# Kernel tuning notes

Measured on AMD Instinct MI355X. Metric: run time of the kernel, lower is better.

Reference implementation:

```python
import jax, jax.numpy as jnp
import numpy as np

L = 4           # num_layers
H = 1536        # hidden_size
NQ = 12         # num_q_heads
NKV = 2         # num_kv_heads
D = 128         # head_dim
I = 8960        # mlp intermediate
S = 2048        # q_len == max_seq_len (full prefill, past_kv_len = 0)
EPS = 1e-6
SCALE = 1.0 / np.sqrt(D)


def setup_inputs() -> dict:
    key = jax.random.key(0)
    ks = jax.random.split(key, 16)
    hidden_states = jax.random.normal(ks[0], (1, S, H), dtype=jnp.float32)
    # real RoPE tables (base 10000), duplicated-half layout like HF Qwen2
    inv_freq = 1.0 / (10000.0 ** (np.arange(0, D, 2, dtype=np.float32) / D))
    t = np.arange(S, dtype=np.float32)
    freqs = np.outer(t, inv_freq)                      # [S, D/2]
    emb = np.concatenate([freqs, freqs], axis=-1)      # [S, D]
    position_cos = jnp.asarray(np.cos(emb))[None]      # [1, S, D]
    position_sin = jnp.asarray(np.sin(emb))[None]
    # causal additive mask [1, 1, S, S]
    causal = jnp.tril(jnp.ones((S, S), dtype=bool))
    attention_mask = jnp.where(causal, 0.0, -1e9).astype(jnp.float32)[None, None]
    sd = 0.02
    Wq = sd * jax.random.normal(ks[1], (L, H, NQ * D), dtype=jnp.float32)
    bq = jnp.zeros((L, NQ * D), dtype=jnp.float32)
    Wk = sd * jax.random.normal(ks[2], (L, H, NKV * D), dtype=jnp.float32)
    bk = jnp.zeros((L, NKV * D), dtype=jnp.float32)
    Wv = sd * jax.random.normal(ks[3], (L, H, NKV * D), dtype=jnp.float32)
    bv = jnp.zeros((L, NKV * D), dtype=jnp.float32)
    Wo = sd * jax.random.normal(ks[4], (L, NQ * D, H), dtype=jnp.float32)
    Wgate = sd * jax.random.normal(ks[5], (L, H, I), dtype=jnp.float32)
    Wup = sd * jax.random.normal(ks[6], (L, H, I), dtype=jnp.float32)
    Wdown = sd * jax.random.normal(ks[7], (L, I, H), dtype=jnp.float32)
    ln1_w = jnp.ones((L, H), dtype=jnp.float32)
    ln2_w = jnp.ones((L, H), dtype=jnp.float32)
    final_ln_w = jnp.ones((H,), dtype=jnp.float32)
    return dict(hidden_states=hidden_states, position_cos=position_cos,
                position_sin=position_sin, attention_mask=attention_mask,
                Wq=Wq, bq=bq, Wk=Wk, bk=bk, Wv=Wv, bv=bv, Wo=Wo,
                Wgate=Wgate, Wup=Wup, Wdown=Wdown,
                ln1_w=ln1_w, ln2_w=ln2_w, final_ln_w=final_ln_w)


def rms_norm(x, w):
    return x * jax.lax.rsqrt(jnp.mean(x * x, axis=-1, keepdims=True) + EPS) * w


def rotate_half(x):
    x1, x2 = jnp.split(x, 2, axis=-1)
    return jnp.concatenate([-x2, x1], axis=-1)


def reference(hidden_states, position_cos, position_sin, attention_mask,
              Wq, bq, Wk, bk, Wv, bv, Wo, Wgate, Wup, Wdown,
              ln1_w, ln2_w, final_ln_w):
    cos = position_cos[:, None]  # [1, 1, S, D]
    sin = position_sin[:, None]
    x = hidden_states
    rep = NQ // NKV
    for i in range(L):
        residual = x
        h = rms_norm(x, ln1_w[i])
        q = (h @ Wq[i] + bq[i]).reshape(1, S, NQ, D).transpose(0, 2, 1, 3)   # [1,NQ,S,D]
        k = (h @ Wk[i] + bk[i]).reshape(1, S, NKV, D).transpose(0, 2, 1, 3)  # [1,NKV,S,D]
        v = (h @ Wv[i] + bv[i]).reshape(1, S, NKV, D).transpose(0, 2, 1, 3)
        q = q * cos + rotate_half(q) * sin
        k = k * cos + rotate_half(k) * sin
        # KV cache write is fp16; full prefill so cache == current k/v (fp16 roundtrip)
        k_full = k.astype(jnp.float16).astype(jnp.float32)
        v_full = v.astype(jnp.float16).astype(jnp.float32)
        k_full = jnp.repeat(k_full, rep, axis=1)  # GQA expand -> [1,NQ,S,D]
        v_full = jnp.repeat(v_full, rep, axis=1)
        scores = jnp.einsum('bhqd,bhkd->bhqk', q, k_full) * SCALE + attention_mask
        probs = jax.nn.softmax(scores, axis=-1)
        attn = jnp.einsum('bhqk,bhkd->bhqd', probs, v_full)
        attn = attn.transpose(0, 2, 1, 3).reshape(1, S, NQ * D)
        x = residual + attn @ Wo[i]
        residual = x
        h = rms_norm(x, ln2_w[i])
        x = residual + (jax.nn.silu(h @ Wgate[i]) * (h @ Wup[i])) @ Wdown[i]
    return rms_norm(x, final_ln_w)
```

## Files before the change

kernel.cpp:

```cpp
#include <hip/hip_runtime.h>

#define S_LEN 2048
#define H_DIM 1536
#define NQ_H 12
#define NKV_H 2
#define HD 128
#define I_DIM 8960
#define QKV_N 2048
#define GU_N 17920
#define SCALE 0.08838834764831845f

typedef _Float16 f16;
typedef _Float16 f16x8 __attribute__((ext_vector_type(8)));
typedef float f32x4 __attribute__((ext_vector_type(4)));

__device__ __forceinline__ void gload16(const void* g, void* l) {
  __builtin_amdgcn_global_load_lds((__attribute__((address_space(1))) void*)g,
                                   (__attribute__((address_space(3))) void*)l,
                                   16, 0, 0);
}

template <int MODE>
__global__ __launch_bounds__(256) void gemm_bt(const f16* __restrict__ A,
                                               const f16* __restrict__ BT,
                                               float* __restrict__ Cf,
                                               f16* __restrict__ Ch,
                                               int M, int N, int K) {
  __shared__ __attribute__((aligned(16))) f16 As[128 * 32];
  __shared__ __attribute__((aligned(16))) f16 Bs[128 * 32];
  const int tid = threadIdx.x;
  const int w = tid >> 6, lane = tid & 63;
  const int quad = lane >> 4, cc = lane & 15;
  const int wm = w >> 1, wn = w & 1;
  const int m0 = blockIdx.y * 128, n0 = blockIdx.x * 128;

  const int c1 = tid, c2 = tid + 256;
  const f16* Ag1 = A + (size_t)(m0 + (c1 >> 2)) * K + (c1 & 3) * 8;
  const f16* Ag2 = A + (size_t)(m0 + (c2 >> 2)) * K + (c2 & 3) * 8;
  const f16* Bg1 = BT + (size_t)(n0 + (c1 >> 2)) * K + (c1 & 3) * 8;
  const f16* Bg2 = BT + (size_t)(n0 + (c2 >> 2)) * K + (c2 & 3) * 8;
  f16* Al1 = As + (w * 64) * 8;
  f16* Al2 = As + (256 + w * 64) * 8;
  f16* Bl1 = Bs + (w * 64) * 8;
  f16* Bl2 = Bs + (256 + w * 64) * 8;

  const f32x4 fz = {0.f, 0.f, 0.f, 0.f};
  f32x4 acc[4][4];
#pragma unroll
  for (int i = 0; i < 4; ++i)
#pragma unroll
    for (int j = 0; j < 4; ++j) acc[i][j] = fz;

  for (int k0 = 0; k0 < K; k0 += 32) {
    __syncthreads();
    gload16(Ag1 + k0, Al1);
    gload16(Ag2 + k0, Al2);
    gload16(Bg1 + k0, Bl1);
    gload16(Bg2 + k0, Bl2);
    __syncthreads();
    f16x8 af[4], bf[4];
#pragma unroll
    for (int i = 0; i < 4; ++i)
      af[i] = *(const f16x8*)(As + (wm * 64 + i * 16 + cc) * 32 + quad * 8);
#pragma unroll
    for (int j = 0; j < 4; ++j)
      bf[j] = *(const f16x8*)(Bs + (wn * 64 + j * 16 + cc) * 32 + quad * 8);
#pragma unroll
    for (int i = 0; i < 4; ++i)
#pragma unroll
      for (int j = 0; j < 4; ++j)
        acc[i][j] = __builtin_amdgcn_mfma_f32_16x16x32_f16(af[i], bf[j], acc[i][j], 0, 0, 0);
  }

#pragma unroll
  for (int i = 0; i < 4; ++i) {
    const int row = m0 + wm * 64 + i * 16 + quad * 4;
#pragma unroll
    for (int j = 0; j < 4; ++j) {
      const int col = n0 + wn * 64 + j * 16 + cc;
#pragma unroll
      for (int r = 0; r < 4; ++r) {
        const size_t idx = (size_t)(row + r) * N + col;
        if (MODE == 0) Cf[idx] = acc[i][j][r];
        else if (MODE == 1) Cf[idx] += acc[i][j][r];
        else Ch[idx] = (f16)acc[i][j][r];
      }
    }
  }
}

__global__ __launch_bounds__(256) void transpose_f2h(const float* __restrict__ src,
                                                     f16* __restrict__ dst,
                                                     int K_, int N_) {
  __shared__ float tile[32][33];
  const int c0 = blockIdx.x * 32, r0 = blockIdx.y * 32;
  const int x = threadIdx.x & 31, y4 = threadIdx.x >> 5;
#pragma unroll
  for (int i = 0; i < 4; ++i) {
    int r = r0 + y4 + i * 8;
    if (r < K_ && c0 + x < N_) tile[y4 + i * 8][x] = src[(size_t)r * N_ + c0 + x];
  }
  __syncthreads();
#pragma unroll
  for (int i = 0; i < 4; ++i) {
    int rr = y4 + i * 8;
    int dr = c0 + rr, dc = r0 + x;
    if (dr < N_ && dc < K_) dst[(size_t)dr * K_ + dc] = (f16)tile[x][rr];
  }
}

template <bool OUT_F32>
__global__ __launch_bounds__(256) void rmsnorm_kernel(const float* __restrict__ x,
                                                      const float* __restrict__ w,
                                                      f16* __restrict__ hh,
                                                      float* __restrict__ hf) {
  const int s = blockIdx.x;
  const float* xr = x + (size_t)s * H_DIM;
  float ss = 0.f;
  for (int i = threadIdx.x; i < H_DIM; i += 256) {
    float v = xr[i];
    ss += v * v;
  }
#pragma unroll
  for (int m = 32; m >= 1; m >>= 1) ss += __shfl_xor(ss, m);
  __shared__ float red[4];
  if ((threadIdx.x & 63) == 0) red[threadIdx.x >> 6] = ss;
  __syncthreads();
  ss = red[0] + red[1] + red[2] + red[3];
  const float rr = rsqrtf(ss * (1.0f / H_DIM) + 1e-6f);
  for (int i = threadIdx.x; i < H_DIM; i += 256) {
    float v = xr[i] * rr * w[i];
    if (OUT_F32) hf[(size_t)s * H_DIM + i] = v;
    else hh[(size_t)s * H_DIM + i] = (f16)v;
  }
}

__global__ __launch_bounds__(256) void rope_kernel(const float* __restrict__ qkv,
                                                   const float* __restrict__ cosb,
                                                   const float* __restrict__ sinb,
                                                   const float* __restrict__ bq,
                                                   const float* __restrict__ bk,
                                                   const float* __restrict__ bv,
                                                   f16* __restrict__ q_r,
                                                   f16* __restrict__ k_r,
                                                   f16* __restrict__ v_r) {
  const int s = blockIdx.x;
  const float* row = qkv + (size_t)s * QKV_N;
#pragma unroll
  for (int ci = 0; ci < 8; ++ci) {
    const int col = ci * 256 + threadIdx.x;
    if (col < 1536) {
      const int hh = col >> 7, d = col & 127;
      const int part = (d < 64) ? d + 64 : d - 64;
      const float v0 = row[col] + bq[col];
      const float v1 = row[(hh << 7) + part] + bq[(hh << 7) + part];
      const float cs = cosb[s * HD + d], sn = sinb[s * HD + d];
      const float rot = (d < 64) ? -v1 : v1;
      q_r[((size_t)hh * S_LEN + s) * HD + d] = (f16)(v0 * cs + rot * sn);
    } else if (col < 1792) {
      const int cc2 = col - 1536;
      const int hh = cc2 >> 7, d = cc2 & 127;
      const int part = (d < 64) ? d + 64 : d - 64;
      const float v0 = row[col] + bk[cc2];
      const float v1 = row[1536 + (hh << 7) + part] + bk[(hh << 7) + part];
      const float cs = cosb[s * HD + d], sn = sinb[s * HD + d];
      const float rot = (d < 64) ? -v1 : v1;
      k_r[((size_t)hh * S_LEN + s) * HD + d] = (f16)(v0 * cs + rot * sn);
    } else {
      const int cc2 = col - 1792;
      const int hh = cc2 >> 7, d = cc2 & 127;
      const float v0 = row[col] + bv[cc2];
      v_r[((size_t)hh * HD + d) * S_LEN + s] = (f16)v0;
    }
  }
}

__global__ __launch_bounds__(256) void attn_kernel(const f16* __restrict__ Q,
                                                   const f16* __restrict__ Kc,
                                                   const f16* __restrict__ Vt,
                                                   f16* __restrict__ Oa) {
  __shared__ __attribute__((aligned(16))) f16 ks[64 * 136];
  __shared__ __attribute__((aligned(16))) f16 vs[128 * 72];
  __shared__ __attribute__((aligned(16))) f16 ps[128 * 72];
  const int h = blockIdx.x, qt = blockIdx.y;
  const int hk = h / (NQ_H / NKV_H);
  const int tid = threadIdx.x, w = tid >> 6, lane = tid & 63;
  const int quad = lane >> 4, cc = lane & 15;

  f16x8 qf[2][4];
  const f16* Qg = Q + ((size_t)h * S_LEN + qt * 128) * HD;
#pragma unroll
  for (int i = 0; i < 2; ++i)
#pragma unroll
    for (int kk = 0; kk < 4; ++kk)
      qf[i][kk] = *(const f16x8*)(Qg + (size_t)(w * 32 + i * 16 + cc) * HD + kk * 32 + quad * 8);

  const f32x4 fz = {0.f, 0.f, 0.f, 0.f};
  f32x4 o_acc[2][8];
  float m_run[2][4], l_run[2][4];
#pragma unroll
  for (int i = 0; i < 2; ++i) {
#pragma unroll
    for (int j = 0; j < 8; ++j) o_acc[i][j] = fz;
#pragma unroll
    for (int r = 0; r < 4; ++r) { m_run[i][r] = -1e30f; l_run[i][r] = 0.f; }
  }

  const int nkt = 2 * qt + 2;
  for (int kt = 0; kt < nkt; ++kt) {
    const int kv0 = kt * 64;
    __syncthreads();
    const f16* Kg = Kc + ((size_t)hk * S_LEN + kv0) * HD;
    for (int t = tid; t < 64 * 16; t += 256) {
      int r = t >> 4, ch = t & 15;
      *(uint4*)(ks + r * 136 + ch * 8) = *(const uint4*)(Kg + (size_t)r * HD + ch * 8);
    }
    const f16* Vg = Vt + (size_t)hk * HD * S_LEN + kv0;
    for (int t = tid; t < 128 * 8; t += 256) {
      int r = t >> 3, ch = t & 7;
      *(uint4*)(vs + r * 72 + ch * 8) = *(const uint4*)(Vg + (size_t)r * S_LEN + ch * 8);
    }
    __syncthreads();

    f32x4 sc[2][4];
#pragma unroll
    for (int i = 0; i < 2; ++i)
#pragma unroll
      for (int j = 0; j < 4; ++j) sc[i][j] = fz;
#pragma unroll
    for (int kk = 0; kk < 4; ++kk) {
      f16x8 bfr[4];
#pragma unroll
      for (int j = 0; j < 4; ++j)
        bfr[j] = *(const f16x8*)(ks + (j * 16 + cc) * 136 + kk * 32 + quad * 8);
#pragma unroll
      for (int i = 0; i < 2; ++i)
#pragma unroll
        for (int j = 0; j < 4; ++j)
          sc[i][j] = __builtin_amdgcn_mfma_f32_16x16x32_f16(qf[i][kk], bfr[j], sc[i][j], 0, 0, 0);
    }

    const bool need_mask = (kv0 + 63) > (qt * 128);
#pragma unroll
    for (int i = 0; i < 2; ++i)
#pragma unroll
      for (int j = 0; j < 4; ++j)
#pragma unroll
        for (int r = 0; r < 4; ++r) {
          float v = sc[i][j][r] * SCALE;
          if (need_mask) {
            int rowg = qt * 128 + w * 32 + i * 16 + quad * 4 + r;
            int colg = kv0 + j * 16 + cc;
            if (colg > rowg) v = -1e30f;
          }
          sc[i][j][r] = v;
        }

#pragma unroll
    for (int i = 0; i < 2; ++i)
#pragma unroll
      for (int r = 0; r < 4; ++r) {
        float mx = sc[i][0][r];
#pragma unroll
        for (int j = 1; j < 4; ++j) mx = fmaxf(mx, sc[i][j][r]);
        mx = fmaxf(mx, __shfl_xor(mx, 1));
        mx = fmaxf(mx, __shfl_xor(mx, 2));
        mx = fmaxf(mx, __shfl_xor(mx, 4));
        mx = fmaxf(mx, __shfl_xor(mx, 8));
        const float mnew = fmaxf(m_run[i][r], mx);
        const float alpha = __expf(m_run[i][r] - mnew);
        m_run[i][r] = mnew;
        l_run[i][r] *= alpha;
#pragma unroll
        for (int jd = 0; jd < 8; ++jd) o_acc[i][jd][r] *= alpha;
        float rs = 0.f;
        const int prow = w * 32 + i * 16 + quad * 4 + r;
#pragma unroll
        for (int j = 0; j < 4; ++j) {
          float p = __expf(sc[i][j][r] - mnew);
          rs += p;
          ps[prow * 72 + j * 16 + cc] = (f16)p;
        }
        rs += __shfl_xor(rs, 1);
        rs += __shfl_xor(rs, 2);
        rs += __shfl_xor(rs, 4);
        rs += __shfl_xor(rs, 8);
        l_run[i][r] += rs;
      }

#pragma unroll
    for (int kk = 0; kk < 2; ++kk) {
      f16x8 pa[2];
#pragma unroll
      for (int i = 0; i < 2; ++i)
        pa[i] = *(const f16x8*)(ps + (w * 32 + i * 16 + cc) * 72 + kk * 32 + quad * 8);
#pragma unroll
      for (int j = 0; j < 8; ++j) {
        f16x8 vb = *(const f16x8*)(vs + (j * 16 + cc) * 72 + kk * 32 + quad * 8);
#pragma unroll
        for (int i = 0; i < 2; ++i)
          o_acc[i][j] = __builtin_amdgcn_mfma_f32_16x16x32_f16(pa[i], vb, o_acc[i][j], 0, 0, 0);
      }
    }
  }

#pragma unroll
  for (int i = 0; i < 2; ++i)
#pragma unroll
    for (int j = 0; j < 8; ++j)
#pragma unroll
      for (int r = 0; r < 4; ++r) {
        const int rowg = qt * 128 + w * 32 + i * 16 + quad * 4 + r;
        const int colg = j * 16 + cc;
        Oa[(size_t)rowg * H_DIM + h * HD + colg] = (f16)(o_acc[i][j][r] / l_run[i][r]);
      }
}

__global__ __launch_bounds__(256) void silu_mul(const f16* __restrict__ gu,
                                                f16* __restrict__ hm) {
  const int i = blockIdx.x * 256 + threadIdx.x;
  const int s = blockIdx.y;
  const float g = (float)gu[(size_t)s * GU_N + i];
  const float u = (float)gu[(size_t)s * GU_N + I_DIM + i];
  const float sig = 1.f / (1.f + __expf(-g));
  hm[(size_t)s * I_DIM + i] = (f16)(g * sig * u);
}

extern "C" void kernel_launch(void* const* d_in, const int* in_sizes, int n_in,
                              void* d_out, int out_size, void* d_ws, size_t ws_size,
                              hipStream_t stream) {
  const float* hidden = (const float*)d_in[0];
  const float* cosb   = (const float*)d_in[1];
  const float* sinb   = (const float*)d_in[2];
  const float* Wq     = (const float*)d_in[4];
  const float* bq     = (const float*)d_in[5];
  const float* Wk     = (const float*)d_in[6];
  const float* bk     = (const float*)d_in[7];
  const float* Wv     = (const float*)d_in[8];
  const float* bv     = (const float*)d_in[9];
  const float* Wo     = (const float*)d_in[10];
  const float* Wg     = (const float*)d_in[11];
  const float* Wu     = (const float*)d_in[12];
  const float* Wd     = (const float*)d_in[13];
  const float* ln1    = (const float*)d_in[14];
  const float* ln2    = (const float*)d_in[15];
  const float* lnf    = (const float*)d_in[16];

  char* wp = (char*)d_ws;
  auto take = [&](size_t bytes) {
    void* p = (void*)wp;
    wp += (bytes + 255) & ~(size_t)255;
    return p;
  };
  f16* wqkvT  = (f16*)take((size_t)QKV_N * H_DIM * 2);
  f16* woT    = (f16*)take((size_t)H_DIM * H_DIM * 2);
  f16* wguT   = (f16*)take((size_t)GU_N * H_DIM * 2);
  f16* wdT    = (f16*)take((size_t)H_DIM * I_DIM * 2);
  float* x    = (float*)take((size_t)S_LEN * H_DIM * 4);
  f16* hbuf   = (f16*)take((size_t)S_LEN * H_DIM * 2);
  float* qkv  = (float*)take((size_t)S_LEN * QKV_N * 4);
  f16* q_r    = (f16*)take((size_t)NQ_H * S_LEN * HD * 2);
  f16* k_r    = (f16*)take((size_t)NKV_H * S_LEN * HD * 2);
  f16* v_r    = (f16*)take((size_t)NKV_H * HD * S_LEN * 2);
  f16* gu     = (f16*)take((size_t)S_LEN * GU_N * 2);
  f16* hmid   = (f16*)take((size_t)S_LEN * I_DIM * 2);

  hipMemcpyAsync(x, hidden, (size_t)S_LEN * H_DIM * 4, hipMemcpyDeviceToDevice, stream);

  for (int l = 0; l < 4; ++l) {
    transpose_f2h<<<dim3(48, 48), 256, 0, stream>>>(Wq + (size_t)l * H_DIM * 1536, wqkvT, H_DIM, 1536);
    transpose_f2h<<<dim3(8, 48), 256, 0, stream>>>(Wk + (size_t)l * H_DIM * 256, wqkvT + (size_t)1536 * H_DIM, H_DIM, 256);
    transpose_f2h<<<dim3(8, 48), 256, 0, stream>>>(Wv + (size_t)l * H_DIM * 256, wqkvT + (size_t)1792 * H_DIM, H_DIM, 256);
    transpose_f2h<<<dim3(48, 48), 256, 0, stream>>>(Wo + (size_t)l * H_DIM * H_DIM, woT, H_DIM, H_DIM);
    transpose_f2h<<<dim3(280, 48), 256, 0, stream>>>(Wg + (size_t)l * H_DIM * I_DIM, wguT, H_DIM, I_DIM);
    transpose_f2h<<<dim3(280, 48), 256, 0, stream>>>(Wu + (size_t)l * H_DIM * I_DIM, wguT + (size_t)I_DIM * H_DIM, H_DIM, I_DIM);
    transpose_f2h<<<dim3(48, 280), 256, 0, stream>>>(Wd + (size_t)l * I_DIM * H_DIM, wdT, I_DIM, H_DIM);

    rmsnorm_kernel<false><<<S_LEN, 256, 0, stream>>>(x, ln1 + l * H_DIM, hbuf, nullptr);
    gemm_bt<0><<<dim3(QKV_N / 128, S_LEN / 128), 256, 0, stream>>>(hbuf, wqkvT, qkv, nullptr, S_LEN, QKV_N, H_DIM);
    rope_kernel<<<S_LEN, 256, 0, stream>>>(qkv, cosb, sinb, bq + l * 1536, bk + l * 256, bv + l * 256, q_r, k_r, v_r);
    attn_kernel<<<dim3(NQ_H, S_LEN / 128), 256, 0, stream>>>(q_r, k_r, v_r, hbuf);
    gemm_bt<1><<<dim3(H_DIM / 128, S_LEN / 128), 256, 0, stream>>>(hbuf, woT, x, nullptr, S_LEN, H_DIM, H_DIM);
    rmsnorm_kernel<false><<<S_LEN, 256, 0, stream>>>(x, ln2 + l * H_DIM, hbuf, nullptr);
    gemm_bt<2><<<dim3(GU_N / 128, S_LEN / 128), 256, 0, stream>>>(hbuf, wguT, nullptr, gu, S_LEN, GU_N, H_DIM);
    silu_mul<<<dim3(I_DIM / 256, S_LEN), 256, 0, stream>>>(gu, hmid);
    gemm_bt<1><<<dim3(H_DIM / 128, S_LEN / 128), 256, 0, stream>>>(hmid, wdT, x, nullptr, S_LEN, H_DIM, I_DIM);
  }
  rmsnorm_kernel<true><<<S_LEN, 256, 0, stream>>>(x, lnf, nullptr, (float*)d_out);
}
```

Baseline: 3.722 ms.

## Add split-K with atomic accumulation for small GEMMs and halve attention query tile

The GEMM kernel gains a split-K dimension via blockIdx.z, with partial results accumulated into fp32 output using atomic adds. QKV, O-projection and down-projection GEMMs use 2 or 4 K-splits, and the QKV output is zeroed first. This targets under-filled grids, where these GEMMs launch only 192-256 blocks on a large GPU. Attention now uses 64-row query tiles with one 16-row fragment per wave, doubling block count and cutting per-block registers. The cost is extra atomic traffic, a memset, and nondeterministic summation order.

```diff
diff --git a/kernel.cpp b/kernel.cpp
--- a/kernel.cpp
+++ b/kernel.cpp
@@ -25,7 +25,7 @@
                                                const f16* __restrict__ BT,
                                                float* __restrict__ Cf,
                                                f16* __restrict__ Ch,
-                                               int M, int N, int K) {
+                                               int N, int Ktot, int Kc) {
   __shared__ __attribute__((aligned(16))) f16 As[128 * 32];
   __shared__ __attribute__((aligned(16))) f16 Bs[128 * 32];
   const int tid = threadIdx.x;
@@ -33,12 +33,13 @@
   const int quad = lane >> 4, cc = lane & 15;
   const int wm = w >> 1, wn = w & 1;
   const int m0 = blockIdx.y * 128, n0 = blockIdx.x * 128;
+  const int kbase = blockIdx.z * Kc;
 
   const int c1 = tid, c2 = tid + 256;
-  const f16* Ag1 = A + (size_t)(m0 + (c1 >> 2)) * K + (c1 & 3) * 8;
-  const f16* Ag2 = A + (size_t)(m0 + (c2 >> 2)) * K + (c2 & 3) * 8;
-  const f16* Bg1 = BT + (size_t)(n0 + (c1 >> 2)) * K + (c1 & 3) * 8;
-  const f16* Bg2 = BT + (size_t)(n0 + (c2 >> 2)) * K + (c2 & 3) * 8;
+  const f16* Ag1 = A + (size_t)(m0 + (c1 >> 2)) * Ktot + kbase + (c1 & 3) * 8;
+  const f16* Ag2 = A + (size_t)(m0 + (c2 >> 2)) * Ktot + kbase + (c2 & 3) * 8;
+  const f16* Bg1 = BT + (size_t)(n0 + (c1 >> 2)) * Ktot + kbase + (c1 & 3) * 8;
+  const f16* Bg2 = BT + (size_t)(n0 + (c2 >> 2)) * Ktot + kbase + (c2 & 3) * 8;
   f16* Al1 = As + (w * 64) * 8;
   f16* Al2 = As + (256 + w * 64) * 8;
   f16* Bl1 = Bs + (w * 64) * 8;
@@ -51,7 +52,7 @@
 #pragma unroll
     for (int j = 0; j < 4; ++j) acc[i][j] = fz;
 
-  for (int k0 = 0; k0 < K; k0 += 32) {
+  for (int k0 = 0; k0 < Kc; k0 += 32) {
     __syncthreads();
     gload16(Ag1 + k0, Al1);
     gload16(Ag2 + k0, Al2);
@@ -81,8 +82,7 @@
 #pragma unroll
       for (int r = 0; r < 4; ++r) {
         const size_t idx = (size_t)(row + r) * N + col;
-        if (MODE == 0) Cf[idx] = acc[i][j][r];
-        else if (MODE == 1) Cf[idx] += acc[i][j][r];
+        if (MODE == 1) unsafeAtomicAdd(&Cf[idx], acc[i][j][r]);
         else Ch[idx] = (f16)acc[i][j][r];
       }
     }
@@ -181,32 +181,27 @@
                                                    f16* __restrict__ Oa) {
   __shared__ __attribute__((aligned(16))) f16 ks[64 * 136];
   __shared__ __attribute__((aligned(16))) f16 vs[128 * 72];
-  __shared__ __attribute__((aligned(16))) f16 ps[128 * 72];
+  __shared__ __attribute__((aligned(16))) f16 ps[64 * 72];
   const int h = blockIdx.x, qt = blockIdx.y;
   const int hk = h / (NQ_H / NKV_H);
   const int tid = threadIdx.x, w = tid >> 6, lane = tid & 63;
   const int quad = lane >> 4, cc = lane & 15;
 
-  f16x8 qf[2][4];
-  const f16* Qg = Q + ((size_t)h * S_LEN + qt * 128) * HD;
-#pragma unroll
-  for (int i = 0; i < 2; ++i)
-#pragma unroll
-    for (int kk = 0; kk < 4; ++kk)
-      qf[i][kk] = *(const f16x8*)(Qg + (size_t)(w * 32 + i * 16 + cc) * HD + kk * 32 + quad * 8);
+  f16x8 qf[4];
+  const f16* Qg = Q + ((size_t)h * S_LEN + qt * 64) * HD;
+#pragma unroll
+  for (int kk = 0; kk < 4; ++kk)
+    qf[kk] = *(const f16x8*)(Qg + (size_t)(w * 16 + cc) * HD + kk * 32 + quad * 8);
 
   const f32x4 fz = {0.f, 0.f, 0.f, 0.f};
-  f32x4 o_acc[2][8];
-  float m_run[2][4], l_run[2][4];
-#pragma unroll
-  for (int i = 0; i < 2; ++i) {
-#pragma unroll
-    for (int j = 0; j < 8; ++j) o_acc[i][j] = fz;
-#pragma unroll
-    for (int r = 0; r < 4; ++r) { m_run[i][r] = -1e30f; l_run[i][r] = 0.f; }
-  }
-
-  const int nkt = 2 * qt + 2;
+  f32x4 o_acc[8];
+  float m_run[4], l_run[4];
+#pragma unroll
+  for (int j = 0; j < 8; ++j) o_acc[j] = fz;
+#pragma unroll
+  for (int r = 0; r < 4; ++r) { m_run[r] = -1e30f; l_run[r] = 0.f; }
+
+  const int nkt = qt + 1;
   for (int kt = 0; kt < nkt; ++kt) {
     const int kv0 = kt * 64;
     __syncthreads();
@@ -222,11 +217,9 @@
     }
     __syncthreads();
 
-    f32x4 sc[2][4];
-#pragma unroll
-    for (int i = 0; i < 2; ++i)
-#pragma unroll
-      for (int j = 0; j < 4; ++j) sc[i][j] = fz;
+    f32x4 sc[4];
+#pragma unroll
+    for (int j = 0; j < 4; ++j) sc[j] = fz;
 #pragma unroll
     for (int kk = 0; kk < 4; ++kk) {
       f16x8 bfr[4];
@@ -234,86 +227,73 @@
       for (int j = 0; j < 4; ++j)
         bfr[j] = *(const f16x8*)(ks + (j * 16 + cc) * 136 + kk * 32 + quad * 8);
 #pragma unroll
-      for (int i = 0; i < 2; ++i)
-#pragma unroll
-        for (int j = 0; j < 4; ++j)
-          sc[i][j] = __builtin_amdgcn_mfma_f32_16x16x32_f16(qf[i][kk], bfr[j], sc[i][j], 0, 0, 0);
-    }
-
-    const bool need_mask = (kv0 + 63) > (qt * 128);
-#pragma unroll
-    for (int i = 0; i < 2; ++i)
-#pragma unroll
       for (int j = 0; j < 4; ++j)
-#pragma unroll
-        for (int r = 0; r < 4; ++r) {
-          float v = sc[i][j][r] * SCALE;
-          if (need_mask) {
-            int rowg = qt * 128 + w * 32 + i * 16 + quad * 4 + r;
-            int colg = kv0 + j * 16 + cc;
-            if (colg > rowg) v = -1e30f;
-          }
-          sc[i][j][r] = v;
+        sc[j] = __builtin_amdgcn_mfma_f32_16x16x32_f16(qf[kk], bfr[j], sc[j], 0, 0, 0);
+    }
+
+    const bool need_mask = (kt == qt);
+#pragma unroll
+    for (int j = 0; j < 4; ++j)
+#pragma unroll
+      for (int r = 0; r < 4; ++r) {
+        float v = sc[j][r] * SCALE;
+        if (need_mask) {
+          int rowg = qt * 64 + w * 16 + quad * 4 + r;
+          int colg = kv0 + j * 16 + cc;
+          if (colg > rowg) v = -1e30f;
         }
-
-#pragma unroll
-    for (int i = 0; i < 2; ++i)
-#pragma unroll
-      for (int r = 0; r < 4; ++r) {
-        float mx = sc[i][0][r];
-#pragma unroll
-        for (int j = 1; j < 4; ++j) mx = fmaxf(mx, sc[i][j][r]);
-        mx = fmaxf(mx, __shfl_xor(mx, 1));
-        mx = fmaxf(mx, __shfl_xor(mx, 2));
-        mx = fmaxf(mx, __shfl_xor(mx, 4));
-        mx = fmaxf(mx, __shfl_xor(mx, 8));
-        const float mnew = fmaxf(m_run[i][r], mx);
-        const float alpha = __expf(m_run[i][r] - mnew);
-        m_run[i][r] = mnew;
-        l_run[i][r] *= alpha;
-#pragma unroll
-        for (int jd = 0; jd < 8; ++jd) o_acc[i][jd][r] *= alpha;
-        float rs = 0.f;
-        const int prow = w * 32 + i * 16 + quad * 4 + r;
-#pragma unroll
-        for (int j = 0; j < 4; ++j) {
-          float p = __expf(sc[i][j][r] - mnew);
-          rs += p;
-          ps[prow * 72 + j * 16 + cc] = (f16)p;
-        }
-        rs += __shfl_xor(rs, 1);
-        rs += __shfl_xor(rs, 2);
-        rs += __shfl_xor(rs, 4);
-        rs += __shfl_xor(rs, 8);
-        l_run[i][r] += rs;
+        sc[j][r] = v;
       }
 
 #pragma unroll
+    for (int r = 0; r < 4; ++r) {
+      float mx = sc[0][r];
+#pragma unroll
+      for (int j = 1; j < 4; ++j) mx = fmaxf(mx, sc[j][r]);
+      mx = fmaxf(mx, __shfl_xor(mx, 1));
+      mx = fmaxf(mx, __shfl_xor(mx, 2));
+      mx = fmaxf(mx, __shfl_xor(mx, 4));
+      mx = fmaxf(mx, __shfl_xor(mx, 8));
+      const float mnew = fmaxf(m_run[r], mx);
+      const float alpha = __expf(m_run[r] - mnew);
+      m_run[r] = mnew;
+      l_run[r] *= alpha;
+#pragma unroll
+      for (int jd = 0; jd < 8; ++jd) o_acc[jd][r] *= alpha;
+      float rs = 0.f;
+      const int prow = w * 16 + quad * 4 + r;
+#pragma unroll
+      for (int j = 0; j < 4; ++j) {
+        float p = __expf(sc[j][r] - mnew);
+        rs += p;
+        ps[prow * 72 + j * 16 + cc] = (f16)p;
+      }
+      rs += __shfl_xor(rs, 1);
+      rs += __shfl_xor(rs, 2);
+      rs += __shfl_xor(rs, 4);
+      rs += __shfl_xor(rs, 8);
+      l_run[r] += rs;
+    }
+
+#pragma unroll
     for (int kk = 0; kk < 2; ++kk) {
-      f16x8 pa[2];
-#pragma unroll
-      for (int i = 0; i < 2; ++i)
-        pa[i] = *(const f16x8*)(ps + (w * 32 + i * 16 + cc) * 72 + kk * 32 + quad * 8);
+      f16x8 pa = *(const f16x8*)(ps + (w * 16 + cc) * 72 + kk * 32 + quad * 8);
 #pragma unroll
       for (int j = 0; j < 8; ++j) {
         f16x8 vb = *(const f16x8*)(vs + (j * 16 + cc) * 72 + kk * 32 + quad * 8);
-#pragma unroll
-        for (int i = 0; i < 2; ++i)
-          o_acc[i][j] = __builtin_amdgcn_mfma_f32_16x16x32_f16(pa[i], vb, o_acc[i][j], 0, 0, 0);
+        o_acc[j] = __builtin_amdgcn_mfma_f32_16x16x32_f16(pa, vb, o_acc[j], 0, 0, 0);
       }
     }
   }
 
 #pragma unroll
-  for (int i = 0; i < 2; ++i)
-#pragma unroll
-    for (int j = 0; j < 8; ++j)
-#pragma unroll
-      for (int r = 0; r < 4; ++r) {
-        const int rowg = qt * 128 + w * 32 + i * 16 + quad * 4 + r;
-        const int colg = j * 16 + cc;
-        Oa[(size_t)rowg * H_DIM + h * HD + colg] = (f16)(o_acc[i][j][r] / l_run[i][r]);
-      }
+  for (int j = 0; j < 8; ++j)
+#pragma unroll
+    for (int r = 0; r < 4; ++r) {
+      const int rowg = qt * 64 + w * 16 + quad * 4 + r;
+      const int colg = j * 16 + cc;
+      Oa[(size_t)rowg * H_DIM + h * HD + colg] = (f16)(o_acc[j][r] / l_run[r]);
+    }
 }
 
 __global__ __launch_bounds__(256) void silu_mul(const f16* __restrict__ gu,
@@ -377,14 +357,15 @@
     transpose_f2h<<<dim3(48, 280), 256, 0, stream>>>(Wd + (size_t)l * I_DIM * H_DIM, wdT, I_DIM, H_DIM);
 
     rmsnorm_kernel<false><<<S_LEN, 256, 0, stream>>>(x, ln1 + l * H_DIM, hbuf, nullptr);
-    gemm_bt<0><<<dim3(QKV_N / 128, S_LEN / 128), 256, 0, stream>>>(hbuf, wqkvT, qkv, nullptr, S_LEN, QKV_N, H_DIM);
+    hipMemsetAsync(qkv, 0, (size_t)S_LEN * QKV_N * 4, stream);
+    gemm_bt<1><<<dim3(QKV_N / 128, S_LEN / 128, 2), 256, 0, stream>>>(hbuf, wqkvT, qkv, nullptr, QKV_N, H_DIM, 768);
     rope_kernel<<<S_LEN, 256, 0, stream>>>(qkv, cosb, sinb, bq + l * 1536, bk + l * 256, bv + l * 256, q_r, k_r, v_r);
-    attn_kernel<<<dim3(NQ_H, S_LEN / 128), 256, 0, stream>>>(q_r, k_r, v_r, hbuf);
-    gemm_bt<1><<<dim3(H_DIM / 128, S_LEN / 128), 256, 0, stream>>>(hbuf, woT, x, nullptr, S_LEN, H_DIM, H_DIM);
+    attn_kernel<<<dim3(NQ_H, S_LEN / 64), 256, 0, stream>>>(q_r, k_r, v_r, hbuf);
+    gemm_bt<1><<<dim3(H_DIM / 128, S_LEN / 128, 4), 256, 0, stream>>>(hbuf, woT, x, nullptr, H_DIM, H_DIM, 384);
     rmsnorm_kernel<false><<<S_LEN, 256, 0, stream>>>(x, ln2 + l * H_DIM, hbuf, nullptr);
-    gemm_bt<2><<<dim3(GU_N / 128, S_LEN / 128), 256, 0, stream>>>(hbuf, wguT, nullptr, gu, S_LEN, GU_N, H_DIM);
+    gemm_bt<2><<<dim3(GU_N / 128, S_LEN / 128, 1), 256, 0, stream>>>(hbuf, wguT, nullptr, gu, GU_N, H_DIM, H_DIM);
     silu_mul<<<dim3(I_DIM / 256, S_LEN), 256, 0, stream>>>(gu, hmid);
-    gemm_bt<1><<<dim3(H_DIM / 128, S_LEN / 128), 256, 0, stream>>>(hmid, wdT, x, nullptr, S_LEN, H_DIM, I_DIM);
+    gemm_bt<1><<<dim3(H_DIM / 128, S_LEN / 128, 4), 256, 0, stream>>>(hmid, wdT, x, nullptr, H_DIM, I_DIM, 2240);
   }
   rmsnorm_kernel<true><<<S_LEN, 256, 0, stream>>>(x, lnf, nullptr, (float*)d_out);
 }
```

Result: faster. 3.094 ms (-16.9%).
